# Optimization experiments

Hardware: AMD Instinct MI355X
Metric: run time of the kernel (lower is better)

The kernel has to match this reference:

```python
import jax, jax.numpy as jnp
import numpy as np

N_NODES = 102400
N_EDGES = 1638400
DIMS = [128, 64, 32, 1]  # decoder_dim=128, decoder_l=3, last layer -> 1


def setup_inputs() -> dict:
    key = jax.random.key(0)
    ks = jax.random.split(key, 10)
    inp = {
        'b_z': jax.random.normal(ks[0], (N_NODES, DIMS[0]), jnp.float32),
        'src': jax.random.randint(ks[1], (N_EDGES,), 0, N_NODES, jnp.int64 if jax.config.jax_enable_x64 else jnp.int32),
        'dst': jax.random.randint(ks[2], (N_EDGES,), 0, N_NODES, jnp.int64 if jax.config.jax_enable_x64 else jnp.int32),
        'edge_weight': jax.random.uniform(ks[3], (N_EDGES,), jnp.float32),
        'b_size': 100,
    }
    # GraphConv weights: W [in, out], bias [out] (DGL xavier init; randn ok for ref)
    for i in range(3):
        inp[f'W{i}'] = jax.random.normal(ks[4 + i], (DIMS[i], DIMS[i + 1]), jnp.float32) * (1.0 / np.sqrt(DIMS[i]))
        inp[f'b{i}'] = jnp.zeros((DIMS[i + 1],), jnp.float32)
    return inp


def _gcn_layer(h, src, dst, ew, W, b, activate):
    n = h.shape[0]
    ones = jnp.ones((src.shape[0],), h.dtype)
    # norm='both': symmetric degree normalization with plain (unweighted) degrees
    out_deg = jnp.clip(jax.ops.segment_sum(ones, src, num_segments=n), 1.0)
    in_deg = jnp.clip(jax.ops.segment_sum(ones, dst, num_segments=n), 1.0)
    h = h * (out_deg ** -0.5)[:, None]
    h = h @ W  # in_feats > out_feats: transform before aggregation (DGL order)
    msg = h[src] * ew[:, None]           # [E, out] edge-weighted gather
    agg = jax.ops.segment_sum(msg, dst, num_segments=n)  # scatter-add
    agg = agg * (in_deg ** -0.5)[:, None] + b
    return jnp.tanh(agg) if activate else agg


def reference(b_z, src, dst, edge_weight, b_size, W0, b0, W1, b1, W2, b2):
    h = b_z
    h = _gcn_layer(h, src, dst, edge_weight, W0, b0, True)
    h = _gcn_layer(h, src, dst, edge_weight, W1, b1, True)
    h = _gcn_layer(h, src, dst, edge_weight, W2, b2, False)
    return h.reshape(b_size, -1)
```

## Files before the change

kernel.cpp:

```cpp
#include <hip/hip_runtime.h>
#include <hip/hip_fp16.h>
#include <math.h>

#define N_NODES 102400
#define N_EDGES 1638400
#define NB 100
#define PB 256
#define EPB (N_EDGES/PB)

union H4 { int2 i2; __half h[4]; };

__global__ __launch_bounds__(256) void histA_kernel(const int* __restrict__ src, const int* __restrict__ dst,
                                                    int* __restrict__ histD, int* __restrict__ outdegCnt) {
    __shared__ int hD[NB];
    int tid = threadIdx.x;
    if (tid < NB) hD[tid] = 0;
    __syncthreads();
    int base = blockIdx.x * EPB;
    for (int i = tid; i < EPB; i += 256) {
        atomicAdd(&hD[dst[base + i] >> 10], 1);
        atomicAdd(&outdegCnt[src[base + i]], 1);
    }
    __syncthreads();
    if (tid < NB) histD[blockIdx.x * NB + tid] = hD[tid];
}

__global__ __launch_bounds__(256) void scanB_kernel(const int* __restrict__ histD,
                                                    int* __restrict__ offD, int* __restrict__ coarseD) {
    __shared__ int totD[NB], baseD[NB + 1];
    int t = threadIdx.x;
    if (t < NB) { int s = 0; for (int k = 0; k < PB; k++) s += histD[k * NB + t]; totD[t] = s; }
    __syncthreads();
    if (t == 0) { int r = 0; for (int j = 0; j < NB; j++) { baseD[j] = r; r += totD[j]; } baseD[NB] = r; }
    __syncthreads();
    if (t < NB) { int r = baseD[t]; for (int k = 0; k < PB; k++) { offD[k * NB + t] = r; r += histD[k * NB + t]; } }
    if (t <= NB) coarseD[t] = baseD[t];
}

__global__ __launch_bounds__(256) void partC_kernel(const int* __restrict__ src, const int* __restrict__ dst,
                                                    const float* __restrict__ ew,
                                                    const int* __restrict__ offD,
                                                    const int* __restrict__ outdegCnt,
                                                    float* __restrict__ outdeg_inv,
                                                    int2* __restrict__ partD) {
    __shared__ int cD[NB];
    int tid = threadIdx.x;
    for (int i = blockIdx.x * 256 + tid; i < N_NODES; i += PB * 256)
        outdeg_inv[i] = 1.0f / sqrtf((float)max(outdegCnt[i], 1));
    if (tid < NB) cD[tid] = offD[blockIdx.x * NB + tid];
    __syncthreads();
    int base = blockIdx.x * EPB;
    for (int i = tid; i < EPB; i += 256) {
        int s = src[base + i], d = dst[base + i];
        float w = ew[base + i];
        int p = atomicAdd(&cD[d >> 10], 1);
        partD[p] = make_int2(s | ((d & 1023) << 17), __float_as_int(w));
    }
}

__global__ __launch_bounds__(1024) void fineD_kernel(const int2* __restrict__ partD, const int* __restrict__ coarseD,
                                                     const float* __restrict__ outdeg_inv,
                                                     int2* __restrict__ edge_perm, int* __restrict__ row_off,
                                                     float* __restrict__ indeg_inv) {
    __shared__ int hist[1024], cursor[1024];
    __shared__ int wsum[16];
    int tid = threadIdx.x, lane = tid & 63, wid = tid >> 6;
    hist[tid] = 0;
    __syncthreads();
    int beg = coarseD[blockIdx.x], end = coarseD[blockIdx.x + 1];
    for (int i = beg + tid; i < end; i += 1024) atomicAdd(&hist[(partD[i].x >> 17) & 1023], 1);
    __syncthreads();
    int v = hist[tid];
    int x = v;
    #pragma unroll
    for (int s = 1; s < 64; s <<= 1) { int t = __shfl_up(x, s, 64); if (lane >= s) x += t; }
    if (lane == 63) wsum[wid] = x;
    __syncthreads();
    if (wid == 0) {
        int ws = (lane < 16) ? wsum[lane] : 0;
        int y = ws;
        #pragma unroll
        for (int s = 1; s < 16; s <<= 1) { int t = __shfl_up(y, s, 64); if (lane >= s) y += t; }
        if (lane < 16) wsum[lane] = y - ws;
    }
    __syncthreads();
    int ex = wsum[wid] + x - v;
    cursor[tid] = beg + ex;
    int node = blockIdx.x * 1024 + tid;
    row_off[node] = beg + ex;
    indeg_inv[node] = 1.0f / sqrtf((float)max(v, 1));
    if (blockIdx.x == NB - 1 && tid == 0) row_off[N_NODES] = N_EDGES;
    __syncthreads();
    for (int i = beg + tid; i < end; i += 1024) {
        int2 t2 = partD[i];
        int d = (t2.x >> 17) & 1023, s = t2.x & 0x1FFFF;
        int p = atomicAdd(&cursor[d], 1);
        float w = __int_as_float(t2.y) * outdeg_inv[s];
        edge_perm[p] = make_int2(s, __float_as_int(w));
    }
}

template<int K, int C, int RN>
__global__ __launch_bounds__(256) void gemm_tile_kernel(
    const float* __restrict__ h, const float* __restrict__ W, __half* __restrict__ out) {
    constexpr int BM = 64;
    constexpr int RM = 4;
    constexpr int KC = 64;
    constexpr int TX = C / RN;
    constexpr int TY = BM / RM;
    static_assert(TX * TY == 256, "bad tile");
    static_assert(RN == 4, "fp16 epilogue assumes RN==4");

    __shared__ float Ws[K * C];
    __shared__ float Hs[KC][BM + 4];

    const int tid = threadIdx.x;
    const long brow = (long)blockIdx.x * BM;

    for (int i = tid; i < K * C; i += 256) Ws[i] = W[i];

    const int tx = tid % TX;
    const int ty = tid / TX;
    float acc[RM][RN] = {};

    const int lr = tid % 16;
    const int lk = tid / 16;

    for (int kc = 0; kc < K; kc += KC) {
        __syncthreads();
        #pragma unroll
        for (int p0 = 0; p0 < BM; p0 += 16) {
            const int r = p0 + lr;
            const float4 hv = *(const float4*)(h + (brow + r) * K + kc + lk * 4);
            Hs[lk * 4 + 0][r] = hv.x;
            Hs[lk * 4 + 1][r] = hv.y;
            Hs[lk * 4 + 2][r] = hv.z;
            Hs[lk * 4 + 3][r] = hv.w;
        }
        __syncthreads();

        #pragma unroll
        for (int k = 0; k < KC; ++k) {
            const float4 a4 = *(const float4*)&Hs[k][ty * RM];
            const float av[RM] = {a4.x, a4.y, a4.z, a4.w};
            float b[RN];
            *(float4*)b = *(const float4*)&Ws[(kc + k) * C + tx * RN];
            #pragma unroll
            for (int i = 0; i < RM; ++i)
                #pragma unroll
                for (int j = 0; j < RN; ++j)
                    acc[i][j] += av[i] * b[j];
        }
    }

    #pragma unroll
    for (int i = 0; i < RM; ++i) {
        const long row = brow + ty * RM + i;
        __half2 p01 = __floats2half2_rn(acc[i][0], acc[i][1]);
        __half2 p23 = __floats2half2_rn(acc[i][2], acc[i][3]);
        int2 packed = make_int2(*(int*)&p01, *(int*)&p23);
        *(int2*)(out + row * C + tx * RN) = packed;
    }
}

__global__ __launch_bounds__(256) void agg64_gemm_kernel(
    const __half* __restrict__ ht, const int* __restrict__ row_off,
    const int2* __restrict__ ep, const float* __restrict__ indeg_inv,
    const float* __restrict__ b0, const float* __restrict__ W1,
    __half* __restrict__ ht1, int N) {
    __shared__ float h1s[8][64];
    const int tid = threadIdx.x;
    const int lane = tid & 63;
    const int wv = tid >> 6;
    const int chunk = lane & 15;
    const int eslot = lane >> 4;
    const int hf = lane >> 5;
    const int c = lane & 31;

    float w1reg[32];
    #pragma unroll
    for (int j = 0; j < 32; ++j) w1reg[j] = W1[(hf * 32 + j) * 32 + c];
    const float bch = b0[(chunk << 2) | eslot];
    const char* htb = (const char*)ht;
    const unsigned coff = (unsigned)(chunk << 3);

    const int pair0 = (blockIdx.x * blockDim.x + tid) >> 6;
    const int npairs = N >> 1;
    const int nwaves = (gridDim.x * blockDim.x) >> 6;

    for (int pid = pair0; pid < npairs; pid += nwaves) {
        const int n0 = pid << 1;
        const int ro0 = row_off[n0], ro1 = row_off[n0 + 1], ro2 = row_off[n0 + 2];
        const int em0 = max(ro1 - 1, 0), em1 = max(ro2 - 1, 0);
        float4 a0 = {0, 0, 0, 0}, a1 = {0, 0, 0, 0};
        float4 c0 = {0, 0, 0, 0}, c1 = {0, 0, 0, 0};
        int e0 = ro0, e1 = ro1;
        while (true) {
            const int i00 = e0 + eslot, i01 = i00 + 4, i02 = i00 + 8, i03 = i00 + 12;
            const int j00 = e1 + eslot, j01 = j00 + 4, j02 = j00 + 8, j03 = j00 + 12;
            int2 p00 = ep[min(i00, em0)];
            int2 p01 = ep[min(i01, em0)];
            int2 p02 = ep[min(i02, em0)];
            int2 p03 = ep[min(i03, em0)];
            int2 p10 = ep[min(j00, em1)];
            int2 p11 = ep[min(j01, em1)];
            int2 p12 = ep[min(j02, em1)];
            int2 p13 = ep[min(j03, em1)];
            float w00 = (i00 < ro1) ? __int_as_float(p00.y) : 0.0f;
            float w01 = (i01 < ro1) ? __int_as_float(p01.y) : 0.0f;
            float w02 = (i02 < ro1) ? __int_as_float(p02.y) : 0.0f;
            float w03 = (i03 < ro1) ? __int_as_float(p03.y) : 0.0f;
            float w10 = (j00 < ro2) ? __int_as_float(p10.y) : 0.0f;
            float w11 = (j01 < ro2) ? __int_as_float(p11.y) : 0.0f;
            float w12 = (j02 < ro2) ? __int_as_float(p12.y) : 0.0f;
            float w13 = (j03 < ro2) ? __int_as_float(p13.y) : 0.0f;
            H4 r00, r01, r02, r03, r10, r11, r12, r13;
            r00.i2 = *(const int2*)(htb + (((unsigned)p00.x << 7) | coff));
            r01.i2 = *(const int2*)(htb + (((unsigned)p01.x << 7) | coff));
            r02.i2 = *(const int2*)(htb + (((unsigned)p02.x << 7) | coff));
            r03.i2 = *(const int2*)(htb + (((unsigned)p03.x << 7) | coff));
            r10.i2 = *(const int2*)(htb + (((unsigned)p10.x << 7) | coff));
            r11.i2 = *(const int2*)(htb + (((unsigned)p11.x << 7) | coff));
            r12.i2 = *(const int2*)(htb + (((unsigned)p12.x << 7) | coff));
            r13.i2 = *(const int2*)(htb + (((unsigned)p13.x << 7) | coff));
            a0.x = fmaf(__half2float(r00.h[0]), w00, a0.x);
            a0.y = fmaf(__half2float(r00.h[1]), w00, a0.y);
            a0.z = fmaf(__half2float(r00.h[2]), w00, a0.z);
            a0.w = fmaf(__half2float(r00.h[3]), w00, a0.w);
            a1.x = fmaf(__half2float(r01.h[0]), w01, a1.x);
            a1.y = fmaf(__half2float(r01.h[1]), w01, a1.y);
            a1.z = fmaf(__half2float(r01.h[2]), w01, a1.z);
            a1.w = fmaf(__half2float(r01.h[3]), w01, a1.w);
            a0.x = fmaf(__half2float(r02.h[0]), w02, a0.x);
            a0.y = fmaf(__half2float(r02.h[1]), w02, a0.y);
            a0.z = fmaf(__half2float(r02.h[2]), w02, a0.z);
            a0.w = fmaf(__half2float(r02.h[3]), w02, a0.w);
            a1.x = fmaf(__half2float(r03.h[0]), w03, a1.x);
            a1.y = fmaf(__half2float(r03.h[1]), w03, a1.y);
            a1.z = fmaf(__half2float(r03.h[2]), w03, a1.z);
            a1.w = fmaf(__half2float(r03.h[3]), w03, a1.w);
            c0.x = fmaf(__half2float(r10.h[0]), w10, c0.x);
            c0.y = fmaf(__half2float(r10.h[1]), w10, c0.y);
            c0.z = fmaf(__half2float(r10.h[2]), w10, c0.z);
            c0.w = fmaf(__half2float(r10.h[3]), w10, c0.w);
            c1.x = fmaf(__half2float(r11.h[0]), w11, c1.x);
            c1.y = fmaf(__half2float(r11.h[1]), w11, c1.y);
            c1.z = fmaf(__half2float(r11.h[2]), w11, c1.z);
            c1.w = fmaf(__half2float(r11.h[3]), w11, c1.w);
            c0.x = fmaf(__half2float(r12.h[0]), w12, c0.x);
            c0.y = fmaf(__half2float(r12.h[1]), w12, c0.y);
            c0.z = fmaf(__half2float(r12.h[2]), w12, c0.z);
            c0.w = fmaf(__half2float(r12.h[3]), w12, c0.w);
            c1.x = fmaf(__half2float(r13.h[0]), w13, c1.x);
            c1.y = fmaf(__half2float(r13.h[1]), w13, c1.y);
            c1.z = fmaf(__half2float(r13.h[2]), w13, c1.z);
            c1.w = fmaf(__half2float(r13.h[3]), w13, c1.w);
            e0 += 16; e1 += 16;
            if (e0 >= ro1 && e1 >= ro2) break;
        }
        a0.x += a1.x; a0.y += a1.y; a0.z += a1.z; a0.w += a1.w;
        c0.x += c1.x; c0.y += c1.y; c0.z += c1.z; c0.w += c1.w;
        #pragma unroll
        for (int s = 16; s <= 32; s <<= 1) {
            a0.x += __shfl_xor(a0.x, s, 64);
            a0.y += __shfl_xor(a0.y, s, 64);
            a0.z += __shfl_xor(a0.z, s, 64);
            a0.w += __shfl_xor(a0.w, s, 64);
            c0.x += __shfl_xor(c0.x, s, 64);
            c0.y += __shfl_xor(c0.y, s, 64);
            c0.z += __shfl_xor(c0.z, s, 64);
            c0.w += __shfl_xor(c0.w, s, 64);
        }
        const float sc0 = indeg_inv[n0], sc1 = indeg_inv[n0 + 1];
        float v0 = (eslot == 0) ? a0.x : (eslot == 1) ? a0.y : (eslot == 2) ? a0.z : a0.w;
        float v1 = (eslot == 0) ? c0.x : (eslot == 1) ? c0.y : (eslot == 2) ? c0.z : c0.w;
        v0 = tanhf(fmaf(v0, sc0, bch));
        v1 = tanhf(fmaf(v1, sc1, bch));
        const int sl = wv << 1;
        h1s[sl][(chunk << 2) | eslot] = v0;
        h1s[sl + 1][(chunk << 2) | eslot] = v1;
        asm volatile("s_waitcnt lgkmcnt(0)" ::: "memory");
        float t0 = 0.0f, t1 = 0.0f;
        #pragma unroll
        for (int j4 = 0; j4 < 8; ++j4) {
            const float4 h0 = *(const float4*)&h1s[sl][hf * 32 + j4 * 4];
            const float4 h1 = *(const float4*)&h1s[sl + 1][hf * 32 + j4 * 4];
            t0 = fmaf(h0.x, w1reg[j4 * 4 + 0], t0);
            t0 = fmaf(h0.y, w1reg[j4 * 4 + 1], t0);
            t0 = fmaf(h0.z, w1reg[j4 * 4 + 2], t0);
            t0 = fmaf(h0.w, w1reg[j4 * 4 + 3], t0);
            t1 = fmaf(h1.x, w1reg[j4 * 4 + 0], t1);
            t1 = fmaf(h1.y, w1reg[j4 * 4 + 1], t1);
            t1 = fmaf(h1.z, w1reg[j4 * 4 + 2], t1);
            t1 = fmaf(h1.w, w1reg[j4 * 4 + 3], t1);
        }
        t0 += __shfl_xor(t0, 32, 64);
        t1 += __shfl_xor(t1, 32, 64);
        if (hf == 0) {
            ht1[(long)n0 * 32 + c] = __float2half_rn(t0);
            ht1[(long)(n0 + 1) * 32 + c] = __float2half_rn(t1);
        }
    }
}

__global__ __launch_bounds__(256) void agg32_dot_kernel(const __half* __restrict__ ht, const int* __restrict__ row_off,
                                 const int2* __restrict__ ep,
                                 const float* __restrict__ indeg_inv, const float* __restrict__ bias,
                                 const float* __restrict__ W2, float* __restrict__ ht2, int N) {
    int quad = (blockIdx.x * blockDim.x + threadIdx.x) >> 6;
    int lane = threadIdx.x & 63;
    int n0 = quad << 2;
    if (n0 >= N) return;
    int chunk = lane & 7;
    int eslot = lane >> 3;
    int ro0 = row_off[n0], ro1 = row_off[n0 + 1], ro2 = row_off[n0 + 2];
    int ro3 = row_off[n0 + 3], ro4 = row_off[n0 + 4];
    int em0 = max(ro1 - 1, 0), em1 = max(ro2 - 1, 0);
    int em2 = max(ro3 - 1, 0), em3 = max(ro4 - 1, 0);
    const char* htb = (const char*)ht;
    unsigned coff = (unsigned)(chunk << 3);
    float4 a0 = {0, 0, 0, 0}, a1 = {0, 0, 0, 0};
    float4 b0 = {0, 0, 0, 0}, b1 = {0, 0, 0, 0};
    float4 c0 = {0, 0, 0, 0}, c1 = {0, 0, 0, 0};
    float4 d0 = {0, 0, 0, 0}, d1 = {0, 0, 0, 0};
    int e0 = ro0, e1 = ro1, e2 = ro2, e3 = ro3;
    while (e0 < ro1 || e1 < ro2 || e2 < ro3 || e3 < ro4) {
        int i00 = e0 + eslot, i01 = i00 + 8;
        int i10 = e1 + eslot, i11 = i10 + 8;
        int i20 = e2 + eslot, i21 = i20 + 8;
        int i30 = e3 + eslot, i31 = i30 + 8;
        int2 p00 = ep[min(i00, em0)];
        int2 p01 = ep[min(i01, em0)];
        int2 p10 = ep[min(i10, em1)];
        int2 p11 = ep[min(i11, em1)];
        int2 p20 = ep[min(i20, em2)];
        int2 p21 = ep[min(i21, em2)];
        int2 p30 = ep[min(i30, em3)];
        int2 p31 = ep[min(i31, em3)];
        float w00 = (i00 < ro1) ? __int_as_float(p00.y) : 0.0f;
        float w01 = (i01 < ro1) ? __int_as_float(p01.y) : 0.0f;
        float w10 = (i10 < ro2) ? __int_as_float(p10.y) : 0.0f;
        float w11 = (i11 < ro2) ? __int_as_float(p11.y) : 0.0f;
        float w20 = (i20 < ro3) ? __int_as_float(p20.y) : 0.0f;
        float w21 = (i21 < ro3) ? __int_as_float(p21.y) : 0.0f;
        float w30 = (i30 < ro4) ? __int_as_float(p30.y) : 0.0f;
        float w31 = (i31 < ro4) ? __int_as_float(p31.y) : 0.0f;
        H4 r00, r01, r10, r11, r20, r21, r30, r31;
        r00.i2 = *(const int2*)(htb + (((unsigned)p00.x << 6) | coff));
        r01.i2 = *(const int2*)(htb + (((unsigned)p01.x << 6) | coff));
        r10.i2 = *(const int2*)(htb + (((unsigned)p10.x << 6) | coff));
        r11.i2 = *(const int2*)(htb + (((unsigned)p11.x << 6) | coff));
        r20.i2 = *(const int2*)(htb + (((unsigned)p20.x << 6) | coff));
        r21.i2 = *(const int2*)(htb + (((unsigned)p21.x << 6) | coff));
        r30.i2 = *(const int2*)(htb + (((unsigned)p30.x << 6) | coff));
        r31.i2 = *(const int2*)(htb + (((unsigned)p31.x << 6) | coff));
        a0.x = fmaf(__half2float(r00.h[0]), w00, a0.x);
        a0.y = fmaf(__half2float(r00.h[1]), w00, a0.y);
        a0.z = fmaf(__half2float(r00.h[2]), w00, a0.z);
        a0.w = fmaf(__half2float(r00.h[3]), w00, a0.w);
        a1.x = fmaf(__half2float(r01.h[0]), w01, a1.x);
        a1.y = fmaf(__half2float(r01.h[1]), w01, a1.y);
        a1.z = fmaf(__half2float(r01.h[2]), w01, a1.z);
        a1.w = fmaf(__half2float(r01.h[3]), w01, a1.w);
        b0.x = fmaf(__half2float(r10.h[0]), w10, b0.x);
        b0.y = fmaf(__half2float(r10.h[1]), w10, b0.y);
        b0.z = fmaf(__half2float(r10.h[2]), w10, b0.z);
        b0.w = fmaf(__half2float(r10.h[3]), w10, b0.w);
        b1.x = fmaf(__half2float(r11.h[0]), w11, b1.x);
        b1.y = fmaf(__half2float(r11.h[1]), w11, b1.y);
        b1.z = fmaf(__half2float(r11.h[2]), w11, b1.z);
        b1.w = fmaf(__half2float(r11.h[3]), w11, b1.w);
        c0.x = fmaf(__half2float(r20.h[0]), w20, c0.x);
        c0.y = fmaf(__half2float(r20.h[1]), w20, c0.y);
        c0.z = fmaf(__half2float(r20.h[2]), w20, c0.z);
        c0.w = fmaf(__half2float(r20.h[3]), w20, c0.w);
        c1.x = fmaf(__half2float(r21.h[0]), w21, c1.x);
        c1.y = fmaf(__half2float(r21.h[1]), w21, c1.y);
        c1.z = fmaf(__half2float(r21.h[2]), w21, c1.z);
        c1.w = fmaf(__half2float(r21.h[3]), w21, c1.w);
        d0.x = fmaf(__half2float(r30.h[0]), w30, d0.x);
        d0.y = fmaf(__half2float(r30.h[1]), w30, d0.y);
        d0.z = fmaf(__half2float(r30.h[2]), w30, d0.z);
        d0.w = fmaf(__half2float(r30.h[3]), w30, d0.w);
        d1.x = fmaf(__half2float(r31.h[0]), w31, d1.x);
        d1.y = fmaf(__half2float(r31.h[1]), w31, d1.y);
        d1.z = fmaf(__half2float(r31.h[2]), w31, d1.z);
        d1.w = fmaf(__half2float(r31.h[3]), w31, d1.w);
        e0 += 16; e1 += 16; e2 += 16; e3 += 16;
    }
    a0.x += a1.x; a0.y += a1.y; a0.z += a1.z; a0.w += a1.w;
    b0.x += b1.x; b0.y += b1.y; b0.z += b1.z; b0.w += b1.w;
    c0.x += c1.x; c0.y += c1.y; c0.z += c1.z; c0.w += c1.w;
    d0.x += d1.x; d0.y += d1.y; d0.z += d1.z; d0.w += d1.w;
    #pragma unroll
    for (int s = 8; s <= 32; s <<= 1) {
        a0.x += __shfl_xor(a0.x, s, 64);
        a0.y += __shfl_xor(a0.y, s, 64);
        a0.z += __shfl_xor(a0.z, s, 64);
        a0.w += __shfl_xor(a0.w, s, 64);
        b0.x += __shfl_xor(b0.x, s, 64);
        b0.y += __shfl_xor(b0.y, s, 64);
        b0.z += __shfl_xor(b0.z, s, 64);
        b0.w += __shfl_xor(b0.w, s, 64);
        c0.x += __shfl_xor(c0.x, s, 64);
        c0.y += __shfl_xor(c0.y, s, 64);
        c0.z += __shfl_xor(c0.z, s, 64);
        c0.w += __shfl_xor(c0.w, s, 64);
        d0.x += __shfl_xor(d0.x, s, 64);
        d0.y += __shfl_xor(d0.y, s, 64);
        d0.z += __shfl_xor(d0.z, s, 64);
        d0.w += __shfl_xor(d0.w, s, 64);
    }
    int q = eslot & 3;
    int ch = (chunk << 2) | q;
    float bb = bias[ch], ww = W2[ch];
    float s0 = indeg_inv[n0], s1 = indeg_inv[n0 + 1], s2 = indeg_inv[n0 + 2], s3 = indeg_inv[n0 + 3];
    float v0 = (q == 0) ? a0.x : (q == 1) ? a0.y : (q == 2) ? a0.z : a0.w;
    float v1 = (q == 0) ? b0.x : (q == 1) ? b0.y : (q == 2) ? b0.z : b0.w;
    float v2 = (q == 0) ? c0.x : (q == 1) ? c0.y : (q == 2) ? c0.z : c0.w;
    float v3 = (q == 0) ? d0.x : (q == 1) ? d0.y : (q == 2) ? d0.z : d0.w;
    float t0 = tanhf(fmaf(v0, s0, bb)) * ww;
    float t1 = tanhf(fmaf(v1, s1, bb)) * ww;
    float t2 = tanhf(fmaf(v2, s2, bb)) * ww;
    float t3 = tanhf(fmaf(v3, s3, bb)) * ww;
    #pragma unroll
    for (int s = 1; s <= 32; s <<= 1) {
        t0 += __shfl_xor(t0, s, 64);
        t1 += __shfl_xor(t1, s, 64);
        t2 += __shfl_xor(t2, s, 64);
        t3 += __shfl_xor(t3, s, 64);
    }
    if (lane == 0) {
        ht2[n0] = 0.5f * t0;
        ht2[n0 + 1] = 0.5f * t1;
        ht2[n0 + 2] = 0.5f * t2;
        ht2[n0 + 3] = 0.5f * t3;
    }
}

__global__ void agg1_kernel(const float* __restrict__ ht2, const int* __restrict__ row_off,
                            const int2* __restrict__ ep,
                            const float* __restrict__ indeg_inv, const float* __restrict__ bias,
                            float* __restrict__ out, int N) {
    int wave = (blockIdx.x * blockDim.x + threadIdx.x) >> 6;
    int lane = threadIdx.x & 63;
    int sub = lane >> 4;
    int slot = lane & 15;
    int node = wave * 4 + sub;
    if (node >= N) return;
    int beg = row_off[node], end = row_off[node + 1];
    float acc = 0.0f;
    for (int e = beg + slot; e < end; e += 16) {
        int2 t = ep[e];
        acc += ht2[t.x] * __int_as_float(t.y);
    }
    #pragma unroll
    for (int s = 1; s <= 8; s <<= 1) acc += __shfl_xor(acc, s, 64);
    if (slot == 0) out[node] = acc * indeg_inv[node] + bias[0];
}

extern "C" void kernel_launch(void* const* d_in, const int* in_sizes, int n_in,
                              void* d_out, int out_size, void* d_ws, size_t ws_size,
                              hipStream_t stream) {
    const float* b_z = (const float*)d_in[0];
    const int*   src = (const int*)d_in[1];
    const int*   dst = (const int*)d_in[2];
    const float* ew  = (const float*)d_in[3];
    const float* W0 = (const float*)d_in[5];
    const float* b0 = (const float*)d_in[6];
    const float* W1 = (const float*)d_in[7];
    const float* b1 = (const float*)d_in[8];
    const float* W2 = (const float*)d_in[9];
    const float* b2 = (const float*)d_in[10];
    float* out = (float*)d_out;

    const int N = N_NODES;
    const int E = N_EDGES;

    char* p = (char*)d_ws;
    int*   row_off    = (int*)p;            p += (size_t)(N + 4) * 4;
    float* outdeg_inv = (float*)p;          p += (size_t)N * 4;
    float* indeg_inv  = (float*)p;          p += (size_t)N * 4;
    int*   histD      = (int*)p;            p += (size_t)PB * NB * 4;
    int*   offD       = (int*)p;            p += (size_t)PB * NB * 4;
    int*   coarseD    = (int*)p;            p += (size_t)(NB + 4) * 4;
    int2*  edge_perm  = (int2*)p;           p += (size_t)E * 8;
    float* bufA       = (float*)p;          p += (size_t)N * 64 * 4;
    float* bufB       = (float*)p;
    int2*   partD     = (int2*)bufA;
    int*    outdegCnt = (int*)bufB;
    __half* ht    = (__half*)bufA;
    __half* ht1   = (__half*)bufB;
    float*  ht2   = bufA;

    hipMemsetAsync(outdegCnt, 0, (size_t)N * 4, stream);
    histA_kernel<<<PB, 256, 0, stream>>>(src, dst, histD, outdegCnt);
    scanB_kernel<<<1, 256, 0, stream>>>(histD, offD, coarseD);
    partC_kernel<<<PB, 256, 0, stream>>>(src, dst, ew, offD, outdegCnt, outdeg_inv, partD);
    fineD_kernel<<<NB, 1024, 0, stream>>>(partD, coarseD, outdeg_inv, edge_perm, row_off, indeg_inv);

    gemm_tile_kernel<128, 64, 4><<<N / 64, 256, 0, stream>>>(b_z, W0, ht);

    agg64_gemm_kernel<<<4096, 256, 0, stream>>>(ht, row_off, edge_perm, indeg_inv, b0, W1, ht1, N);

    agg32_dot_kernel<<<N / 16, 256, 0, stream>>>(ht1, row_off, edge_perm, indeg_inv, b1, W2, ht2, N);

    agg1_kernel<<<N / 16, 256, 0, stream>>>(ht2, row_off, edge_perm, indeg_inv, b2, out, N);
}
```

Measured before the change: 374.8 us.

## Fuse histogram pass with first GEMM and compute out-degrees via partitioned histogram

Merges the edge-histogram pass and the first dense transform into one launch, with the histogram blocks and GEMM tiles sharing one grid, so the GEMM overlaps the graph preprocessing. It also replaces the global atomic out-degree counting (and its memset) with a coarse/fine bucketed histogram over source nodes: partC writes a 16-bit partS array and a new fineS kernel counts it in shared memory. This removes contended global atomics at the cost of an extra kernel launch, an extra partition write stream and a larger workspace.

```diff
diff --git a/kernel.cpp b/kernel.cpp
--- a/kernel.cpp
+++ b/kernel.cpp
@@ -10,44 +10,104 @@
 
 union H4 { int2 i2; __half h[4]; };
 
-__global__ __launch_bounds__(256) void histA_kernel(const int* __restrict__ src, const int* __restrict__ dst,
-                                                    int* __restrict__ histD, int* __restrict__ outdegCnt) {
-    __shared__ int hD[NB];
-    int tid = threadIdx.x;
-    if (tid < NB) hD[tid] = 0;
-    __syncthreads();
-    int base = blockIdx.x * EPB;
-    for (int i = tid; i < EPB; i += 256) {
-        atomicAdd(&hD[dst[base + i] >> 10], 1);
-        atomicAdd(&outdegCnt[src[base + i]], 1);
-    }
-    __syncthreads();
-    if (tid < NB) histD[blockIdx.x * NB + tid] = hD[tid];
-}
-
-__global__ __launch_bounds__(256) void scanB_kernel(const int* __restrict__ histD,
-                                                    int* __restrict__ offD, int* __restrict__ coarseD) {
-    __shared__ int totD[NB], baseD[NB + 1];
+__global__ __launch_bounds__(256) void fusedA_kernel(
+    const int* __restrict__ src, const int* __restrict__ dst,
+    int* __restrict__ histD, int* __restrict__ histS,
+    const float* __restrict__ h, const float* __restrict__ W, __half* __restrict__ out) {
+    constexpr int K = 128, C = 64, BM = 64, RM = 4, RN = 4, KC = 64, TX = 16;
+    __shared__ __align__(16) char smem[(K * C + KC * (BM + 4)) * 4];
+    const int tid = threadIdx.x;
+
+    if (blockIdx.x < PB) {
+        int* hD = (int*)smem;
+        int* hS = hD + 128;
+        if (tid < NB) { hD[tid] = 0; hS[tid] = 0; }
+        __syncthreads();
+        int base = blockIdx.x * EPB;
+        for (int i = tid; i < EPB; i += 256) {
+            atomicAdd(&hD[dst[base + i] >> 10], 1);
+            atomicAdd(&hS[src[base + i] >> 10], 1);
+        }
+        __syncthreads();
+        if (tid < NB) {
+            histD[blockIdx.x * NB + tid] = hD[tid];
+            histS[blockIdx.x * NB + tid] = hS[tid];
+        }
+        return;
+    }
+
+    float* Ws = (float*)smem;
+    float* Hs = Ws + K * C;
+    const long brow = (long)(blockIdx.x - PB) * BM;
+
+    for (int i = tid; i < K * C; i += 256) Ws[i] = W[i];
+
+    const int tx = tid % TX;
+    const int ty = tid / TX;
+    float acc[RM][RN] = {};
+    const int lr = tid % 16;
+    const int lk = tid / 16;
+
+    for (int kc = 0; kc < K; kc += KC) {
+        __syncthreads();
+        #pragma unroll
+        for (int p0 = 0; p0 < BM; p0 += 16) {
+            const int r = p0 + lr;
+            const float4 hv = *(const float4*)(h + (brow + r) * K + kc + lk * 4);
+            Hs[(lk * 4 + 0) * (BM + 4) + r] = hv.x;
+            Hs[(lk * 4 + 1) * (BM + 4) + r] = hv.y;
+            Hs[(lk * 4 + 2) * (BM + 4) + r] = hv.z;
+            Hs[(lk * 4 + 3) * (BM + 4) + r] = hv.w;
+        }
+        __syncthreads();
+        #pragma unroll
+        for (int k = 0; k < KC; ++k) {
+            const float4 a4 = *(const float4*)&Hs[k * (BM + 4) + ty * RM];
+            const float av[RM] = {a4.x, a4.y, a4.z, a4.w};
+            float b[RN];
+            *(float4*)b = *(const float4*)&Ws[(kc + k) * C + tx * RN];
+            #pragma unroll
+            for (int i = 0; i < RM; ++i)
+                #pragma unroll
+                for (int j = 0; j < RN; ++j)
+                    acc[i][j] += av[i] * b[j];
+        }
+    }
+
+    #pragma unroll
+    for (int i = 0; i < RM; ++i) {
+        const long row = brow + ty * RM + i;
+        __half2 p01 = __floats2half2_rn(acc[i][0], acc[i][1]);
+        __half2 p23 = __floats2half2_rn(acc[i][2], acc[i][3]);
+        int2 packed = make_int2(*(int*)&p01, *(int*)&p23);
+        *(int2*)(out + row * C + tx * RN) = packed;
+    }
+}
+
+__global__ __launch_bounds__(256) void scanB_kernel(const int* __restrict__ histD, const int* __restrict__ histS,
+                                                    int* __restrict__ offD, int* __restrict__ offS,
+                                                    int* __restrict__ coarseD, int* __restrict__ coarseS) {
+    __shared__ int totD[NB], totS[NB], baseD[NB + 1], baseS[NB + 1];
     int t = threadIdx.x;
     if (t < NB) { int s = 0; for (int k = 0; k < PB; k++) s += histD[k * NB + t]; totD[t] = s; }
-    __syncthreads();
-    if (t == 0) { int r = 0; for (int j = 0; j < NB; j++) { baseD[j] = r; r += totD[j]; } baseD[NB] = r; }
+    else if (t >= 128 && t < 128 + NB) { int j = t - 128; int s = 0; for (int k = 0; k < PB; k++) s += histS[k * NB + j]; totS[j] = s; }
+    __syncthreads();
+    if (t == 0)   { int r = 0; for (int j = 0; j < NB; j++) { baseD[j] = r; r += totD[j]; } baseD[NB] = r; }
+    if (t == 128) { int r = 0; for (int j = 0; j < NB; j++) { baseS[j] = r; r += totS[j]; } baseS[NB] = r; }
     __syncthreads();
     if (t < NB) { int r = baseD[t]; for (int k = 0; k < PB; k++) { offD[k * NB + t] = r; r += histD[k * NB + t]; } }
+    else if (t >= 128 && t < 128 + NB) { int j = t - 128; int r = baseS[j]; for (int k = 0; k < PB; k++) { offS[k * NB + j] = r; r += histS[k * NB + j]; } }
     if (t <= NB) coarseD[t] = baseD[t];
+    if (t >= 128 && t <= 128 + NB) coarseS[t - 128] = baseS[t - 128];
 }
 
 __global__ __launch_bounds__(256) void partC_kernel(const int* __restrict__ src, const int* __restrict__ dst,
                                                     const float* __restrict__ ew,
-                                                    const int* __restrict__ offD,
-                                                    const int* __restrict__ outdegCnt,
-                                                    float* __restrict__ outdeg_inv,
-                                                    int2* __restrict__ partD) {
-    __shared__ int cD[NB];
+                                                    const int* __restrict__ offD, const int* __restrict__ offS,
+                                                    int2* __restrict__ partD, unsigned short* __restrict__ partS) {
+    __shared__ int cD[NB], cS[NB];
     int tid = threadIdx.x;
-    for (int i = blockIdx.x * 256 + tid; i < N_NODES; i += PB * 256)
-        outdeg_inv[i] = 1.0f / sqrtf((float)max(outdegCnt[i], 1));
-    if (tid < NB) cD[tid] = offD[blockIdx.x * NB + tid];
+    if (tid < NB) { cD[tid] = offD[blockIdx.x * NB + tid]; cS[tid] = offS[blockIdx.x * NB + tid]; }
     __syncthreads();
     int base = blockIdx.x * EPB;
     for (int i = tid; i < EPB; i += 256) {
@@ -55,7 +115,21 @@
         float w = ew[base + i];
         int p = atomicAdd(&cD[d >> 10], 1);
         partD[p] = make_int2(s | ((d & 1023) << 17), __float_as_int(w));
-    }
+        int q = atomicAdd(&cS[s >> 10], 1);
+        partS[q] = (unsigned short)(s & 1023);
+    }
+}
+
+__global__ __launch_bounds__(1024) void fineS_kernel(const unsigned short* __restrict__ partS, const int* __restrict__ coarseS,
+                                                     float* __restrict__ outdeg_inv) {
+    __shared__ int hist[1024];
+    int tid = threadIdx.x;
+    hist[tid] = 0;
+    __syncthreads();
+    int beg = coarseS[blockIdx.x], end = coarseS[blockIdx.x + 1];
+    for (int i = beg + tid; i < end; i += 1024) atomicAdd(&hist[partS[i]], 1);
+    __syncthreads();
+    outdeg_inv[blockIdx.x * 1024 + tid] = 1.0f / sqrtf((float)max(hist[tid], 1));
 }
 
 __global__ __launch_bounds__(1024) void fineD_kernel(const int2* __restrict__ partD, const int* __restrict__ coarseD,
@@ -97,69 +171,6 @@
         int p = atomicAdd(&cursor[d], 1);
         float w = __int_as_float(t2.y) * outdeg_inv[s];
         edge_perm[p] = make_int2(s, __float_as_int(w));
-    }
-}
-
-template<int K, int C, int RN>
-__global__ __launch_bounds__(256) void gemm_tile_kernel(
-    const float* __restrict__ h, const float* __restrict__ W, __half* __restrict__ out) {
-    constexpr int BM = 64;
-    constexpr int RM = 4;
-    constexpr int KC = 64;
-    constexpr int TX = C / RN;
-    constexpr int TY = BM / RM;
-    static_assert(TX * TY == 256, "bad tile");
-    static_assert(RN == 4, "fp16 epilogue assumes RN==4");
-
-    __shared__ float Ws[K * C];
-    __shared__ float Hs[KC][BM + 4];
-
-    const int tid = threadIdx.x;
-    const long brow = (long)blockIdx.x * BM;
-
-    for (int i = tid; i < K * C; i += 256) Ws[i] = W[i];
-
-    const int tx = tid % TX;
-    const int ty = tid / TX;
-    float acc[RM][RN] = {};
-
-    const int lr = tid % 16;
-    const int lk = tid / 16;
-
-    for (int kc = 0; kc < K; kc += KC) {
-        __syncthreads();
-        #pragma unroll
-        for (int p0 = 0; p0 < BM; p0 += 16) {
-            const int r = p0 + lr;
-            const float4 hv = *(const float4*)(h + (brow + r) * K + kc + lk * 4);
-            Hs[lk * 4 + 0][r] = hv.x;
-            Hs[lk * 4 + 1][r] = hv.y;
-            Hs[lk * 4 + 2][r] = hv.z;
-            Hs[lk * 4 + 3][r] = hv.w;
-        }
-        __syncthreads();
-
-        #pragma unroll
-        for (int k = 0; k < KC; ++k) {
-            const float4 a4 = *(const float4*)&Hs[k][ty * RM];
-            const float av[RM] = {a4.x, a4.y, a4.z, a4.w};
-            float b[RN];
-            *(float4*)b = *(const float4*)&Ws[(kc + k) * C + tx * RN];
-            #pragma unroll
-            for (int i = 0; i < RM; ++i)
-                #pragma unroll
-                for (int j = 0; j < RN; ++j)
-                    acc[i][j] += av[i] * b[j];
-        }
-    }
-
-    #pragma unroll
-    for (int i = 0; i < RM; ++i) {
-        const long row = brow + ty * RM + i;
-        __half2 p01 = __floats2half2_rn(acc[i][0], acc[i][1]);
-        __half2 p23 = __floats2half2_rn(acc[i][2], acc[i][3]);
-        int2 packed = make_int2(*(int*)&p01, *(int*)&p23);
-        *(int2*)(out + row * C + tx * RN) = packed;
     }
 }
 
@@ -482,25 +493,28 @@
     float* outdeg_inv = (float*)p;          p += (size_t)N * 4;
     float* indeg_inv  = (float*)p;          p += (size_t)N * 4;
     int*   histD      = (int*)p;            p += (size_t)PB * NB * 4;
+    int*   histS      = (int*)p;            p += (size_t)PB * NB * 4;
     int*   offD       = (int*)p;            p += (size_t)PB * NB * 4;
+    int*   offS       = (int*)p;            p += (size_t)PB * NB * 4;
     int*   coarseD    = (int*)p;            p += (size_t)(NB + 4) * 4;
+    int*   coarseS    = (int*)p;            p += (size_t)(NB + 4) * 4;
     int2*  edge_perm  = (int2*)p;           p += (size_t)E * 8;
-    float* bufA       = (float*)p;          p += (size_t)N * 64 * 4;
-    float* bufB       = (float*)p;
-    int2*   partD     = (int2*)bufA;
-    int*    outdegCnt = (int*)bufB;
-    __half* ht    = (__half*)bufA;
-    __half* ht1   = (__half*)bufB;
-    float*  ht2   = bufA;
-
-    hipMemsetAsync(outdegCnt, 0, (size_t)N * 4, stream);
-    histA_kernel<<<PB, 256, 0, stream>>>(src, dst, histD, outdegCnt);
-    scanB_kernel<<<1, 256, 0, stream>>>(histD, offD, coarseD);
-    partC_kernel<<<PB, 256, 0, stream>>>(src, dst, ew, offD, outdegCnt, outdeg_inv, partD);
+    char*  bufP       = p;                  p += (size_t)E * 8;
+    char*  bufS       = p;                  p += (size_t)E * 2;
+    char*  bufH       = p;
+    int2*           partD = (int2*)bufP;
+    __half*         ht1   = (__half*)bufP;
+    unsigned short* partS = (unsigned short*)bufS;
+    float*          ht2   = (float*)bufS;
+    __half*         ht    = (__half*)bufH;
+
+    fusedA_kernel<<<PB + N / 64, 256, 0, stream>>>(src, dst, histD, histS, b_z, W0, ht);
+
+    scanB_kernel<<<1, 256, 0, stream>>>(histD, histS, offD, offS, coarseD, coarseS);
+    partC_kernel<<<PB, 256, 0, stream>>>(src, dst, ew, offD, offS, partD, partS);
+    fineS_kernel<<<NB, 1024, 0, stream>>>(partS, coarseS, outdeg_inv);
     fineD_kernel<<<NB, 1024, 0, stream>>>(partD, coarseD, outdeg_inv, edge_perm, row_off, indeg_inv);
 
-    gemm_tile_kernel<128, 64, 4><<<N / 64, 256, 0, stream>>>(b_z, W0, ht);
-
     agg64_gemm_kernel<<<4096, 256, 0, stream>>>(ht, row_off, edge_perm, indeg_inv, b0, W1, ht1, N);
 
     agg32_dot_kernel<<<N / 16, 256, 0, stream>>>(ht1, row_off, edge_perm, indeg_inv, b1, W2, ht2, N);
```

Measured after the change: 329.4 us. -12.1%, faster.
